# Performance work log

Measured on AMD Instinct MI355X. Metric: run time of the kernel, lower is better.

The kernel has to match this reference:

```python
import jax, jax.numpy as jnp
import numpy as np

NUM_LAYERS = 3
EPS = 1e-12  # torch F.normalize eps

NU, NI, D = 200000, 100000, 64
E = 2000000
B = 8192


def setup_inputs() -> dict:
    key = jax.random.key(0)
    ks = jax.random.split(key, 7)
    # Xavier-uniform embeddings (fan_in = num_nodes, fan_out = D)
    def xavier(k, n, d):
        bound = np.sqrt(6.0 / (n + d))
        return jax.random.uniform(k, (n, d), jnp.float32, -bound, bound)
    return {
        "user_feat": xavier(ks[0], NU, D),
        "item_feat": xavier(ks[1], NI, D),
        "edge_u": jax.random.randint(ks[2], (E,), 0, NU, jnp.int32),
        "edge_i": jax.random.randint(ks[3], (E,), 0, NI, jnp.int32),
        "users": jax.random.randint(ks[4], (B,), 0, NU, jnp.int32),
        "pos_items": jax.random.randint(ks[5], (B,), 0, NI, jnp.int32),
        "neg_items": jax.random.randint(ks[6], (B,), 0, NI, jnp.int32),
    }


def _l2norm(h):
    n = jnp.sqrt(jnp.sum(h * h, axis=1, keepdims=True))
    return h / jnp.maximum(n, EPS)


def reference(user_feat, item_feat, edge_u, edge_i, users, pos_items, neg_items):
    Nu, Ni = user_feat.shape[0], item_feat.shape[0]
    ones = jnp.ones(edge_u.shape[0], jnp.float32)
    # symmetric degree norm, identical for both edge directions
    deg_u = jax.ops.segment_sum(ones, edge_u, num_segments=Nu)
    deg_i = jax.ops.segment_sum(ones, edge_i, num_segments=Ni)
    norm = (deg_u[edge_u] * deg_i[edge_i]) ** -0.5  # [E]
    norm = norm[:, None]  # [E,1]

    uh, ih = user_feat, item_feat
    ue, ie = user_feat, item_feat
    for k in range(NUM_LAYERS):
        # gather-scale-scatter for both edge directions using pre-layer feats
        new_ih = jax.ops.segment_sum(norm * uh[edge_u], edge_i, num_segments=Ni)
        new_uh = jax.ops.segment_sum(norm * ih[edge_i], edge_u, num_segments=Nu)
        uh, ih = _l2norm(new_uh), _l2norm(new_ih)
        ue = ue + uh * (1.0 / (k + 1))
        ie = ie + ih * (1.0 / (k + 1))

    return ue[users], ie[pos_items], ie[neg_items]
```

## Files before the change

### kernel.cpp

```cpp
#include <hip/hip_runtime.h>
#include <math.h>


__device__ __forceinline__ unsigned short f2bf(float f) {
    unsigned int b = __float_as_uint(f);
    b += 0x7FFFu + ((b >> 16) & 1u);
    return (unsigned short)(b >> 16);
}
__device__ __forceinline__ float bf2f(unsigned short u) {
    return __uint_as_float(((unsigned int)u) << 16);
}

__global__ void count_deg_kernel(const int* __restrict__ eu, const int* __restrict__ ei,
                                 int* __restrict__ deg, int E, int NU) {
    int e = blockIdx.x * blockDim.x + threadIdx.x;
    if (e >= E) return;
    atomicAdd(&deg[eu[e]], 1);
    atomicAdd(&deg[NU + ei[e]], 1);
}

__global__ void bump_kernel(const int* __restrict__ deg, int* __restrict__ offs,
                            int* __restrict__ cursor, float* __restrict__ isd,
                            int* __restrict__ total, int n) {
    int i = blockIdx.x * blockDim.x + threadIdx.x;
    if (i >= n) return;
    int d = deg[i];
    int o = atomicAdd(total, d);
    offs[i] = o;
    cursor[i] = o;
    isd[i] = d > 0 ? rsqrtf((float)d) : 0.f;
}

__global__ void conv_bf16_kernel(const float* __restrict__ src,
                                 unsigned short* __restrict__ dst, int n4) {
    int t = blockIdx.x * blockDim.x + threadIdx.x;
    if (t >= n4) return;
    float4 f = ((const float4*)src)[t];
    ushort4 o;
    o.x = f2bf(f.x); o.y = f2bf(f.y); o.z = f2bf(f.z); o.w = f2bf(f.w);
    ((ushort4*)dst)[t] = o;
}

__global__ void fill_csr_kernel(const int* __restrict__ eu, const int* __restrict__ ei,
                                const float* __restrict__ isd,
                                int* __restrict__ cursor, int2* __restrict__ csr,
                                int E, int NU) {
    int t = blockIdx.x * blockDim.x + threadIdx.x;
    if (t < E) {
        int u = eu[t], v = ei[t];
        float w = isd[u] * isd[NU + v];
        csr[atomicAdd(&cursor[u], 1)] = make_int2(v, __float_as_int(w));
    } else if (t < 2 * E) {
        int e = t - E;
        int u = eu[e], v = ei[e];
        float w = isd[u] * isd[NU + v];
        csr[atomicAdd(&cursor[NU + v], 1)] = make_int2(u, __float_as_int(w));
    }
}

__device__ __forceinline__ float4 gather_row(const unsigned short* __restrict__ sfeat,
                                             const int2* __restrict__ csr,
                                             int start, int dcount, int g, int l16) {
    float4 a0 = make_float4(0.f, 0.f, 0.f, 0.f);
    float4 a1 = make_float4(0.f, 0.f, 0.f, 0.f);
    int j = g;
    for (; j + 4 < dcount; j += 8) {
        int2 e0 = csr[start + j];
        int2 e1 = csr[start + j + 4];
        float w0 = __int_as_float(e0.y);
        float w1 = __int_as_float(e1.y);
        ushort4 f0 = *(const ushort4*)(sfeat + (size_t)e0.x * 64 + l16 * 4);
        ushort4 f1 = *(const ushort4*)(sfeat + (size_t)e1.x * 64 + l16 * 4);
        a0.x = fmaf(w0, bf2f(f0.x), a0.x); a0.y = fmaf(w0, bf2f(f0.y), a0.y);
        a0.z = fmaf(w0, bf2f(f0.z), a0.z); a0.w = fmaf(w0, bf2f(f0.w), a0.w);
        a1.x = fmaf(w1, bf2f(f1.x), a1.x); a1.y = fmaf(w1, bf2f(f1.y), a1.y);
        a1.z = fmaf(w1, bf2f(f1.z), a1.z); a1.w = fmaf(w1, bf2f(f1.w), a1.w);
    }
    if (j < dcount) {
        int2 e0 = csr[start + j];
        float w0 = __int_as_float(e0.y);
        ushort4 f0 = *(const ushort4*)(sfeat + (size_t)e0.x * 64 + l16 * 4);
        a0.x = fmaf(w0, bf2f(f0.x), a0.x); a0.y = fmaf(w0, bf2f(f0.y), a0.y);
        a0.z = fmaf(w0, bf2f(f0.z), a0.z); a0.w = fmaf(w0, bf2f(f0.w), a0.w);
    }
    float4 a = make_float4(a0.x + a1.x, a0.y + a1.y, a0.z + a1.z, a0.w + a1.w);
    #pragma unroll
    for (int m = 16; m <= 32; m <<= 1) {
        a.x += __shfl_xor(a.x, m, 64);
        a.y += __shfl_xor(a.y, m, 64);
        a.z += __shfl_xor(a.z, m, 64);
        a.w += __shfl_xor(a.w, m, 64);
    }
    float ss = a.x * a.x + a.y * a.y + a.z * a.z + a.w * a.w;
    #pragma unroll
    for (int m = 1; m <= 8; m <<= 1) ss += __shfl_xor(ss, m, 64);
    float scale = 1.f / fmaxf(sqrtf(ss), 1e-12f);
    a.x *= scale; a.y *= scale; a.z *= scale; a.w *= scale;
    return a;
}

__global__ void prop_both_kernel(const unsigned short* __restrict__ uc,
                                 const unsigned short* __restrict__ ic,
                                 unsigned short* __restrict__ ud,
                                 unsigned short* __restrict__ id,
                                 const int* __restrict__ offs, const int* __restrict__ deg,
                                 const int2* __restrict__ csr, int NU, int NT) {
    int wave = blockIdx.x * (blockDim.x >> 6) + (threadIdx.x >> 6);
    if (wave >= NT) return;
    int lane = threadIdx.x & 63;
    int g = lane >> 4, l16 = lane & 15;
    int r = __builtin_amdgcn_readfirstlane(wave);
    const unsigned short* sfeat;
    unsigned short* dst;
    if (r < NU) { sfeat = ic; dst = ud + (size_t)r * 64; }
    else        { sfeat = uc; dst = id + (size_t)(r - NU) * 64; }
    int start  = __builtin_amdgcn_readfirstlane(offs[r]);
    int dcount = __builtin_amdgcn_readfirstlane(deg[r]);
    float4 a = gather_row(sfeat, csr, start, dcount, g, l16);
    if (g == 0) {
        ushort4 o;
        o.x = f2bf(a.x); o.y = f2bf(a.y); o.z = f2bf(a.z); o.w = f2bf(a.w);
        *(ushort4*)(dst + l16 * 4) = o;
    }
}

__global__ void final_kernel(const float* __restrict__ user_feat,
                             const float* __restrict__ item_feat,
                             const unsigned short* __restrict__ uhA,
                             const unsigned short* __restrict__ ihA,
                             const unsigned short* __restrict__ uhB,
                             const unsigned short* __restrict__ ihB,
                             const int* __restrict__ users, const int* __restrict__ pos,
                             const int* __restrict__ neg,
                             const int* __restrict__ offs, const int* __restrict__ deg,
                             const int2* __restrict__ csr, float* __restrict__ out,
                             int NU, int B) {
    int wave = blockIdx.x * (blockDim.x >> 6) + (threadIdx.x >> 6);
    if (wave >= 3 * B) return;
    int lane = threadIdx.x & 63;
    int g = lane >> 4, l16 = lane & 15;
    int seg = wave / B, b = wave - seg * B;
    int r, idx;
    const unsigned short *sfeat, *h1, *h2;
    const float* orig;
    if (seg == 0) {
        idx = users[b]; r = idx;
        sfeat = ihB; orig = user_feat; h1 = uhA; h2 = uhB;
    } else {
        idx = (seg == 1) ? pos[b] : neg[b];
        r = NU + idx;
        sfeat = uhB; orig = item_feat; h1 = ihA; h2 = ihB;
    }
    r = __builtin_amdgcn_readfirstlane(r);
    int start  = __builtin_amdgcn_readfirstlane(offs[r]);
    int dcount = __builtin_amdgcn_readfirstlane(deg[r]);
    float4 a = gather_row(sfeat, csr, start, dcount, g, l16);
    if (g == 0) {
        float4 o = *(const float4*)(orig + (size_t)idx * 64 + l16 * 4);
        ushort4 v1 = *(const ushort4*)(h1 + (size_t)idx * 64 + l16 * 4);
        ushort4 v2 = *(const ushort4*)(h2 + (size_t)idx * 64 + l16 * 4);
        const float c3 = 1.0f / 3.0f;
        o.x += bf2f(v1.x) + 0.5f * bf2f(v2.x) + c3 * a.x;
        o.y += bf2f(v1.y) + 0.5f * bf2f(v2.y) + c3 * a.y;
        o.z += bf2f(v1.z) + 0.5f * bf2f(v2.z) + c3 * a.z;
        o.w += bf2f(v1.w) + 0.5f * bf2f(v2.w) + c3 * a.w;
        *(float4*)(out + (size_t)wave * 64 + l16 * 4) = o;
    }
}

extern "C" void kernel_launch(void* const* d_in, const int* in_sizes, int n_in,
                              void* d_out, int out_size, void* d_ws, size_t ws_size,
                              hipStream_t stream) {
    const float* user_feat = (const float*)d_in[0];
    const float* item_feat = (const float*)d_in[1];
    const int* edge_u = (const int*)d_in[2];
    const int* edge_i = (const int*)d_in[3];
    const int* users  = (const int*)d_in[4];
    const int* pos    = (const int*)d_in[5];
    const int* neg    = (const int*)d_in[6];
    float* out = (float*)d_out;

    const int D = 64;
    const int NU = in_sizes[0] / D;
    const int NI = in_sizes[1] / D;
    const int E  = in_sizes[2];
    const int B  = in_sizes[4];
    const int NT = NU + NI;

    char* ws = (char*)d_ws;
    size_t off = 0;
    auto alloc = [&](size_t bytes) -> void* {
        void* p = ws + off;
        off += bytes;
        off = (off + 255) & ~(size_t)255;
        return p;
    };
    size_t zbytes = (size_t)(NT + 1) * 4;
    char* zbase = (char*)alloc(zbytes);
    int* deg   = (int*)zbase;
    int* total = deg + NT;
    int*   offs   = (int*)alloc((size_t)NT * 4);
    int*   cursor = (int*)alloc((size_t)NT * 4);
    float* isd    = (float*)alloc((size_t)NT * 4);
    int2*  csr    = (int2*)alloc((size_t)2 * E * 8);
    unsigned short* ufb = (unsigned short*)alloc((size_t)NU * D * 2);
    unsigned short* ifb = (unsigned short*)alloc((size_t)NI * D * 2);
    unsigned short* uhA = (unsigned short*)alloc((size_t)NU * D * 2);
    unsigned short* ihA = (unsigned short*)alloc((size_t)NI * D * 2);
    unsigned short* uhB = (unsigned short*)alloc((size_t)NU * D * 2);
    unsigned short* ihB = (unsigned short*)alloc((size_t)NI * D * 2);

    hipMemsetAsync(zbase, 0, zbytes, stream);

    const int tb = 256;
    count_deg_kernel<<<(E + tb - 1) / tb, tb, 0, stream>>>(edge_u, edge_i, deg, E, NU);
    bump_kernel<<<(NT + tb - 1) / tb, tb, 0, stream>>>(deg, offs, cursor, isd, total, NT);

    int n4u = NU * D / 4, n4i = NI * D / 4;
    conv_bf16_kernel<<<(n4u + tb - 1) / tb, tb, 0, stream>>>(user_feat, ufb, n4u);
    conv_bf16_kernel<<<(n4i + tb - 1) / tb, tb, 0, stream>>>(item_feat, ifb, n4i);

    fill_csr_kernel<<<(2 * E + tb - 1) / tb, tb, 0, stream>>>(edge_u, edge_i, isd,
                                                              cursor, csr, E, NU);

    prop_both_kernel<<<(NT + 3) / 4, tb, 0, stream>>>(ufb, ifb, uhA, ihA,
                                                      offs, deg, csr, NU, NT);
    prop_both_kernel<<<(NT + 3) / 4, tb, 0, stream>>>(uhA, ihA, uhB, ihB,
                                                      offs, deg, csr, NU, NT);
    final_kernel<<<(3 * B + 3) / 4, tb, 0, stream>>>(
        user_feat, item_feat, uhA, ihA, uhB, ihB,
        users, pos, neg, offs, deg, csr, out, NU, B);
}
```

Measured before the change: 786.5 us.

## Map each destination row to a 16-lane group instead of a full wavefront

The row-gather kernels now give each 16-lane group its own destination row, so one wavefront handles four rows, where before the whole 64-lane wave split one row's edges four ways and then reduced across lanes. The edge loop is unrolled by four with four accumulators per lane to keep several gathers in flight, and the cross-group shuffle reduction goes away. In exchange, row metadata is no longer wave-uniform (readfirstlane is dropped), and rows of different degree within one wave cause divergence, though average degree here is about 13-20.

```diff
diff --git a/kernel.cpp b/kernel.cpp
--- a/kernel.cpp
+++ b/kernel.cpp
@@ -58,39 +58,45 @@
     }
 }
 
-__device__ __forceinline__ float4 gather_row(const unsigned short* __restrict__ sfeat,
-                                             const int2* __restrict__ csr,
-                                             int start, int dcount, int g, int l16) {
+__device__ __forceinline__ float4 gather16(const unsigned short* __restrict__ sfeat,
+                                           const int2* __restrict__ csr,
+                                           int start, int dcount, int l16) {
     float4 a0 = make_float4(0.f, 0.f, 0.f, 0.f);
     float4 a1 = make_float4(0.f, 0.f, 0.f, 0.f);
-    int j = g;
-    for (; j + 4 < dcount; j += 8) {
+    float4 a2 = make_float4(0.f, 0.f, 0.f, 0.f);
+    float4 a3 = make_float4(0.f, 0.f, 0.f, 0.f);
+    int j = 0;
+    for (; j + 3 < dcount; j += 4) {
         int2 e0 = csr[start + j];
-        int2 e1 = csr[start + j + 4];
-        float w0 = __int_as_float(e0.y);
-        float w1 = __int_as_float(e1.y);
+        int2 e1 = csr[start + j + 1];
+        int2 e2 = csr[start + j + 2];
+        int2 e3 = csr[start + j + 3];
         ushort4 f0 = *(const ushort4*)(sfeat + (size_t)e0.x * 64 + l16 * 4);
         ushort4 f1 = *(const ushort4*)(sfeat + (size_t)e1.x * 64 + l16 * 4);
+        ushort4 f2 = *(const ushort4*)(sfeat + (size_t)e2.x * 64 + l16 * 4);
+        ushort4 f3 = *(const ushort4*)(sfeat + (size_t)e3.x * 64 + l16 * 4);
+        float w0 = __int_as_float(e0.y), w1 = __int_as_float(e1.y);
+        float w2 = __int_as_float(e2.y), w3 = __int_as_float(e3.y);
         a0.x = fmaf(w0, bf2f(f0.x), a0.x); a0.y = fmaf(w0, bf2f(f0.y), a0.y);
         a0.z = fmaf(w0, bf2f(f0.z), a0.z); a0.w = fmaf(w0, bf2f(f0.w), a0.w);
         a1.x = fmaf(w1, bf2f(f1.x), a1.x); a1.y = fmaf(w1, bf2f(f1.y), a1.y);
         a1.z = fmaf(w1, bf2f(f1.z), a1.z); a1.w = fmaf(w1, bf2f(f1.w), a1.w);
-    }
-    if (j < dcount) {
+        a2.x = fmaf(w2, bf2f(f2.x), a2.x); a2.y = fmaf(w2, bf2f(f2.y), a2.y);
+        a2.z = fmaf(w2, bf2f(f2.z), a2.z); a2.w = fmaf(w2, bf2f(f2.w), a2.w);
+        a3.x = fmaf(w3, bf2f(f3.x), a3.x); a3.y = fmaf(w3, bf2f(f3.y), a3.y);
+        a3.z = fmaf(w3, bf2f(f3.z), a3.z); a3.w = fmaf(w3, bf2f(f3.w), a3.w);
+    }
+    for (; j < dcount; ++j) {
         int2 e0 = csr[start + j];
         float w0 = __int_as_float(e0.y);
         ushort4 f0 = *(const ushort4*)(sfeat + (size_t)e0.x * 64 + l16 * 4);
         a0.x = fmaf(w0, bf2f(f0.x), a0.x); a0.y = fmaf(w0, bf2f(f0.y), a0.y);
         a0.z = fmaf(w0, bf2f(f0.z), a0.z); a0.w = fmaf(w0, bf2f(f0.w), a0.w);
     }
-    float4 a = make_float4(a0.x + a1.x, a0.y + a1.y, a0.z + a1.z, a0.w + a1.w);
-    #pragma unroll
-    for (int m = 16; m <= 32; m <<= 1) {
-        a.x += __shfl_xor(a.x, m, 64);
-        a.y += __shfl_xor(a.y, m, 64);
-        a.z += __shfl_xor(a.z, m, 64);
-        a.w += __shfl_xor(a.w, m, 64);
-    }
+    float4 a = make_float4(a0.x + a1.x + a2.x + a3.x,
+                           a0.y + a1.y + a2.y + a3.y,
+                           a0.z + a1.z + a2.z + a3.z,
+                           a0.w + a1.w + a2.w + a3.w);
     float ss = a.x * a.x + a.y * a.y + a.z * a.z + a.w * a.w;
     #pragma unroll
     for (int m = 1; m <= 8; m <<= 1) ss += __shfl_xor(ss, m, 64);
@@ -105,23 +111,20 @@
                                  unsigned short* __restrict__ id,
                                  const int* __restrict__ offs, const int* __restrict__ deg,
                                  const int2* __restrict__ csr, int NU, int NT) {
-    int wave = blockIdx.x * (blockDim.x >> 6) + (threadIdx.x >> 6);
-    if (wave >= NT) return;
-    int lane = threadIdx.x & 63;
-    int g = lane >> 4, l16 = lane & 15;
-    int r = __builtin_amdgcn_readfirstlane(wave);
+    int t = blockIdx.x * blockDim.x + threadIdx.x;
+    int r = t >> 4;
+    if (r >= NT) return;
+    int l16 = t & 15;
     const unsigned short* sfeat;
     unsigned short* dst;
     if (r < NU) { sfeat = ic; dst = ud + (size_t)r * 64; }
     else        { sfeat = uc; dst = id + (size_t)(r - NU) * 64; }
-    int start  = __builtin_amdgcn_readfirstlane(offs[r]);
-    int dcount = __builtin_amdgcn_readfirstlane(deg[r]);
-    float4 a = gather_row(sfeat, csr, start, dcount, g, l16);
-    if (g == 0) {
-        ushort4 o;
-        o.x = f2bf(a.x); o.y = f2bf(a.y); o.z = f2bf(a.z); o.w = f2bf(a.w);
-        *(ushort4*)(dst + l16 * 4) = o;
-    }
+    int start  = offs[r];
+    int dcount = deg[r];
+    float4 a = gather16(sfeat, csr, start, dcount, l16);
+    ushort4 o;
+    o.x = f2bf(a.x); o.y = f2bf(a.y); o.z = f2bf(a.z); o.w = f2bf(a.w);
+    *(ushort4*)(dst + l16 * 4) = o;
 }
 
 __global__ void final_kernel(const float* __restrict__ user_feat,
@@ -135,11 +138,11 @@
                              const int* __restrict__ offs, const int* __restrict__ deg,
                              const int2* __restrict__ csr, float* __restrict__ out,
                              int NU, int B) {
-    int wave = blockIdx.x * (blockDim.x >> 6) + (threadIdx.x >> 6);
-    if (wave >= 3 * B) return;
-    int lane = threadIdx.x & 63;
-    int g = lane >> 4, l16 = lane & 15;
-    int seg = wave / B, b = wave - seg * B;
+    int t = blockIdx.x * blockDim.x + threadIdx.x;
+    int s = t >> 4;
+    if (s >= 3 * B) return;
+    int l16 = t & 15;
+    int seg = s / B, b = s - seg * B;
     int r, idx;
     const unsigned short *sfeat, *h1, *h2;
     const float* orig;
@@ -151,21 +154,18 @@
         r = NU + idx;
         sfeat = uhB; orig = item_feat; h1 = ihA; h2 = ihB;
     }
-    r = __builtin_amdgcn_readfirstlane(r);
-    int start  = __builtin_amdgcn_readfirstlane(offs[r]);
-    int dcount = __builtin_amdgcn_readfirstlane(deg[r]);
-    float4 a = gather_row(sfeat, csr, start, dcount, g, l16);
-    if (g == 0) {
-        float4 o = *(const float4*)(orig + (size_t)idx * 64 + l16 * 4);
-        ushort4 v1 = *(const ushort4*)(h1 + (size_t)idx * 64 + l16 * 4);
-        ushort4 v2 = *(const ushort4*)(h2 + (size_t)idx * 64 + l16 * 4);
-        const float c3 = 1.0f / 3.0f;
-        o.x += bf2f(v1.x) + 0.5f * bf2f(v2.x) + c3 * a.x;
-        o.y += bf2f(v1.y) + 0.5f * bf2f(v2.y) + c3 * a.y;
-        o.z += bf2f(v1.z) + 0.5f * bf2f(v2.z) + c3 * a.z;
-        o.w += bf2f(v1.w) + 0.5f * bf2f(v2.w) + c3 * a.w;
-        *(float4*)(out + (size_t)wave * 64 + l16 * 4) = o;
-    }
+    int start  = offs[r];
+    int dcount = deg[r];
+    float4 a = gather16(sfeat, csr, start, dcount, l16);
+    float4 o = *(const float4*)(orig + (size_t)idx * 64 + l16 * 4);
+    ushort4 v1 = *(const ushort4*)(h1 + (size_t)idx * 64 + l16 * 4);
+    ushort4 v2 = *(const ushort4*)(h2 + (size_t)idx * 64 + l16 * 4);
+    const float c3 = 1.0f / 3.0f;
+    o.x += bf2f(v1.x) + 0.5f * bf2f(v2.x) + c3 * a.x;
+    o.y += bf2f(v1.y) + 0.5f * bf2f(v2.y) + c3 * a.y;
+    o.z += bf2f(v1.z) + 0.5f * bf2f(v2.z) + c3 * a.z;
+    o.w += bf2f(v1.w) + 0.5f * bf2f(v2.w) + c3 * a.w;
+    *(float4*)(out + (size_t)s * 64 + l16 * 4) = o;
 }
 
 extern "C" void kernel_launch(void* const* d_in, const int* in_sizes, int n_in,
@@ -223,11 +223,13 @@
     fill_csr_kernel<<<(2 * E + tb - 1) / tb, tb, 0, stream>>>(edge_u, edge_i, isd,
                                                               cursor, csr, E, NU);
 
-    prop_both_kernel<<<(NT + 3) / 4, tb, 0, stream>>>(ufb, ifb, uhA, ihA,
-                                                      offs, deg, csr, NU, NT);
-    prop_both_kernel<<<(NT + 3) / 4, tb, 0, stream>>>(uhA, ihA, uhB, ihB,
-                                                      offs, deg, csr, NU, NT);
-    final_kernel<<<(3 * B + 3) / 4, tb, 0, stream>>>(
+    int pthreads = NT * 16;
+    prop_both_kernel<<<(pthreads + tb - 1) / tb, tb, 0, stream>>>(
+        ufb, ifb, uhA, ihA, offs, deg, csr, NU, NT);
+    prop_both_kernel<<<(pthreads + tb - 1) / tb, tb, 0, stream>>>(
+        uhA, ihA, uhB, ihB, offs, deg, csr, NU, NT);
+    int fthreads = 3 * B * 16;
+    final_kernel<<<(fthreads + tb - 1) / tb, tb, 0, stream>>>(
         user_feat, item_feat, uhA, ihA, uhB, ihB,
         users, pos, neg, offs, deg, csr, out, NU, B);
 }
```

New measurement: 704.1 us. -10.5%, faster.
